# Kernel tuning notes

Hardware: AMD Instinct MI355X
Metric: run time of the kernel (lower is better)

The kernel has to match this reference:

```python
import jax, jax.numpy as jnp
import numpy as np

NEG_INF = -9.0e15  # matches torch's -9000000000000000.0 mask value
ALPHA = 0.2        # leaky_relu negative slope
F_OUT = 128


def setup_inputs() -> dict:
    key = jax.random.key(0)
    k1, k2, k3, k4 = jax.random.split(key, 4)
    B, N, F_IN = 4, 4096, 128
    x = jax.random.normal(k1, (B, N, F_IN), dtype=jnp.float32)
    adj = jax.random.randint(k2, (B, N, N), 0, 2, dtype=jnp.int32)
    # xavier-uniform-like init for params
    lim_W = float(np.sqrt(6.0 / (F_IN + F_OUT)))
    W = jax.random.uniform(k3, (F_IN, F_OUT), jnp.float32, -lim_W, lim_W)
    lim_a = float(np.sqrt(6.0 / (2 * F_OUT + 1)))
    a = jax.random.uniform(k4, (2 * F_OUT, 1), jnp.float32, -lim_a, lim_a)
    return {"x": x, "adj": adj, "W": W, "a": a}


def reference(x, adj, W, a):
    # x: [B, N, Fin], adj: [B, N, N], W: [Fin, Fout], a: [2*Fout, 1]
    Wh = jnp.matmul(x, W)                       # [B, N, Fout]
    Wh1 = jnp.matmul(Wh, a[:F_OUT, :])          # [B, N, 1]
    Wh2 = jnp.matmul(Wh, a[F_OUT:, :])          # [B, N, 1]
    # NOTE: faithful to the source: e = Wh1 + Wh2 is [B, N, 1] (no transpose)
    e = jax.nn.leaky_relu(Wh1 + Wh2, negative_slope=ALPHA)
    # broadcast e across last dim of adj, mask, row-softmax over axis 2
    scores = jnp.where(adj > 0, e, jnp.float32(NEG_INF))  # [B, N, N]
    attention = jax.nn.softmax(scores, axis=2)
    # dropout with p=0.0 / eval mode -> identity
    h_prime = jnp.matmul(attention, Wh)         # [B, N, Fout]
    return h_prime
```

## Files before the change

kernel.cpp:

```cpp
#include <hip/hip_runtime.h>
#include <hip/hip_bf16.h>

typedef unsigned short u16;
typedef unsigned int u32;
typedef short bf16x8 __attribute__((ext_vector_type(8)));
typedef float f32x4 __attribute__((ext_vector_type(4)));

__device__ inline float bf2f(u16 u) { return __uint_as_float(((u32)u) << 16); }
__device__ inline u16 f2bf(float f) {
    u32 x = __float_as_uint(f);
    return (u16)((x + 0x7FFFu + ((x >> 16) & 1u)) >> 16);
}

__global__ __launch_bounds__(256) void k_gemm1(const float* __restrict__ x,
                                               const float* __restrict__ W,
                                               u16* __restrict__ Wht,
                                               float* __restrict__ S) {
    __shared__ __align__(16) u16 Wt[128][136];
    const int t = threadIdx.x;
    {
        int k = t >> 1;
        int f0 = (t & 1) * 64;
        const float4* wp = reinterpret_cast<const float4*>(W + k * 128 + f0);
#pragma unroll
        for (int q = 0; q < 16; ++q) {
            float4 v = wp[q];
            int f = f0 + q * 4;
            Wt[f + 0][k] = f2bf(v.x);
            Wt[f + 1][k] = f2bf(v.y);
            Wt[f + 2][k] = f2bf(v.z);
            Wt[f + 3][k] = f2bf(v.w);
        }
    }
    __syncthreads();

    const int w = t >> 6, l = t & 63;
    const int lr = l & 15, lg = l >> 4;
    const int fh = (w & 1) * 64;
    const int jh = (w >> 1) * 64;
    const int j0 = blockIdx.x * 128;

    f32x4 acc[4][4];
#pragma unroll
    for (int m = 0; m < 4; ++m)
#pragma unroll
        for (int n = 0; n < 4; ++n) acc[m][n] = (f32x4){0.f, 0.f, 0.f, 0.f};

#pragma unroll
    for (int ks = 0; ks < 4; ++ks) {
        bf16x8 a[4], bb[4];
#pragma unroll
        for (int m = 0; m < 4; ++m)
            a[m] = *reinterpret_cast<const bf16x8*>(&Wt[fh + m * 16 + lr][ks * 32 + lg * 8]);
#pragma unroll
        for (int n = 0; n < 4; ++n) {
            int j = j0 + jh + n * 16 + lr;
            const float* xp = x + (size_t)j * 128 + ks * 32 + lg * 8;
            float4 v0 = *reinterpret_cast<const float4*>(xp);
            float4 v1 = *reinterpret_cast<const float4*>(xp + 4);
            bf16x8 bv;
            bv[0] = (short)f2bf(v0.x); bv[1] = (short)f2bf(v0.y);
            bv[2] = (short)f2bf(v0.z); bv[3] = (short)f2bf(v0.w);
            bv[4] = (short)f2bf(v1.x); bv[5] = (short)f2bf(v1.y);
            bv[6] = (short)f2bf(v1.z); bv[7] = (short)f2bf(v1.w);
            bb[n] = bv;
        }
#pragma unroll
        for (int m = 0; m < 4; ++m)
#pragma unroll
            for (int n = 0; n < 4; ++n)
                acc[m][n] = __builtin_amdgcn_mfma_f32_16x16x32_bf16(a[m], bb[n], acc[m][n], 0, 0, 0);
    }

    const int bb_ = blockIdx.x >> 5;
    const int jj = (blockIdx.x & 31) * 128;
    u16* base = Wht + ((size_t)bb_ << 19);
    float* Sb = S + bb_ * 128;
#pragma unroll
    for (int m = 0; m < 4; ++m) {
        int f = fh + m * 16 + lg * 4;
#pragma unroll
        for (int n = 0; n < 4; ++n) {
            int j = jj + jh + n * 16 + lr;
#pragma unroll
            for (int r = 0; r < 4; ++r)
                base[(size_t)(f + r) * 4096 + j] = f2bf(acc[m][n][r]);
        }
#pragma unroll
        for (int r = 0; r < 4; ++r) {
            float sj = 0.f;
#pragma unroll
            for (int n = 0; n < 4; ++n) sj += acc[m][n][r];
            sj += __shfl_xor(sj, 1);
            sj += __shfl_xor(sj, 2);
            sj += __shfl_xor(sj, 4);
            sj += __shfl_xor(sj, 8);
            if (lr == 0) atomicAdd(&Sb[f + r], sj);
        }
    }
}

__global__ __launch_bounds__(256) void k_gemm2(const int* __restrict__ adj,
                                               const u16* __restrict__ Wht,
                                               float* __restrict__ part,
                                               int* __restrict__ cnt) {
    __shared__ __align__(16) u16 As[2][64][72];

    const int t = threadIdx.x;
    const int raw = blockIdx.x;
    const int swz = (raw & 7) * 64 + (raw >> 3);
    const int b   = swz >> 7;
    const int ksp = (swz >> 6) & 1;
    const int i0  = (swz & 63) * 64;
    const int koff = ksp * 2048;

    const int* adjb = adj + ((size_t)b << 24) + (size_t)i0 * 4096 + koff;
    const u16* whb  = Wht + ((size_t)b << 19) + koff;

    const int ai = t >> 2;
    const int aq = t & 3;
    const int* aptr = adjb + (size_t)ai * 4096 + aq * 16;

    int4 av[4];
    int cntv = 0;

    auto issueA = [&](int kt) {
        const int4* p = reinterpret_cast<const int4*>(aptr + kt * 64);
        av[0] = p[0]; av[1] = p[1]; av[2] = p[2]; av[3] = p[3];
    };
    auto convertA = [&](int buf) {
        u32 u[8];
#pragma unroll
        for (int q = 0; q < 4; ++q) {
            int4 v = av[q];
            cntv += (v.x > 0) + (v.y > 0) + (v.z > 0) + (v.w > 0);
            u[q * 2 + 0] = ((v.x > 0) ? 0x3F80u : 0u) | (((v.y > 0) ? 0x3F80u : 0u) << 16);
            u[q * 2 + 1] = ((v.z > 0) ? 0x3F80u : 0u) | (((v.w > 0) ? 0x3F80u : 0u) << 16);
        }
        *reinterpret_cast<uint4*>(&As[buf][ai][aq * 16]) = make_uint4(u[0], u[1], u[2], u[3]);
        *reinterpret_cast<uint4*>(&As[buf][ai][aq * 16 + 8]) = make_uint4(u[4], u[5], u[6], u[7]);
    };

    const int w = t >> 6, l = t & 63;
    const int lr = l & 15, lg = l >> 4;
    const int ir0 = (w & 1) * 2;
    const int fr0 = (w >> 1) * 4;

    const u16* bptr0 = whb + (size_t)((fr0 + 0) * 16 + lr) * 4096 + lg * 8;
    const u16* bptr1 = whb + (size_t)((fr0 + 1) * 16 + lr) * 4096 + lg * 8;
    const u16* bptr2 = whb + (size_t)((fr0 + 2) * 16 + lr) * 4096 + lg * 8;
    const u16* bptr3 = whb + (size_t)((fr0 + 3) * 16 + lr) * 4096 + lg * 8;

    f32x4 acc[2][4];
#pragma unroll
    for (int m = 0; m < 2; ++m)
#pragma unroll
        for (int n = 0; n < 4; ++n) acc[m][n] = (f32x4){0.f, 0.f, 0.f, 0.f};

    issueA(0);
    convertA(0);
    __syncthreads();

    for (int kt = 0; kt < 32; ++kt) {
        const int cur = kt & 1;
        bf16x8 bb0[4], bb1[4];
        bb0[0] = *reinterpret_cast<const bf16x8*>(bptr0 + kt * 64);
        bb0[1] = *reinterpret_cast<const bf16x8*>(bptr1 + kt * 64);
        bb0[2] = *reinterpret_cast<const bf16x8*>(bptr2 + kt * 64);
        bb0[3] = *reinterpret_cast<const bf16x8*>(bptr3 + kt * 64);
        bb1[0] = *reinterpret_cast<const bf16x8*>(bptr0 + kt * 64 + 32);
        bb1[1] = *reinterpret_cast<const bf16x8*>(bptr1 + kt * 64 + 32);
        bb1[2] = *reinterpret_cast<const bf16x8*>(bptr2 + kt * 64 + 32);
        bb1[3] = *reinterpret_cast<const bf16x8*>(bptr3 + kt * 64 + 32);
        if (kt + 1 < 32) issueA(kt + 1);

#pragma unroll
        for (int ks = 0; ks < 2; ++ks) {
            bf16x8 a0 = *reinterpret_cast<const bf16x8*>(&As[cur][(ir0 + 0) * 16 + lr][ks * 32 + lg * 8]);
            bf16x8 a1 = *reinterpret_cast<const bf16x8*>(&As[cur][(ir0 + 1) * 16 + lr][ks * 32 + lg * 8]);
#pragma unroll
            for (int n = 0; n < 4; ++n) {
                bf16x8 bv = ks ? bb1[n] : bb0[n];
                acc[0][n] = __builtin_amdgcn_mfma_f32_16x16x32_bf16(a0, bv, acc[0][n], 0, 0, 0);
                acc[1][n] = __builtin_amdgcn_mfma_f32_16x16x32_bf16(a1, bv, acc[1][n], 0, 0, 0);
            }
        }

        if (kt + 1 < 32) convertA(cur ^ 1);
        __syncthreads();
    }

    int c = cntv + __shfl_xor(cntv, 1);
    c += __shfl_xor(c, 2);
    if ((t & 3) == 0) atomicAdd(&cnt[b * 4096 + i0 + ai], c);

    float* pb = part + ((size_t)ksp << 21) + ((size_t)b * 4096 + i0) * 128;
#pragma unroll
    for (int m = 0; m < 2; ++m) {
#pragma unroll
        for (int n = 0; n < 4; ++n) {
            int f = (fr0 + n) * 16 + lr;
#pragma unroll
            for (int r = 0; r < 4; ++r) {
                int il = (ir0 + m) * 16 + lg * 4 + r;
                pb[(size_t)il * 128 + f] = acc[m][n][r];
            }
        }
    }
}

__global__ __launch_bounds__(256) void k_fin(const float* __restrict__ part,
                                             const int* __restrict__ cnt,
                                             const float* __restrict__ S,
                                             float* __restrict__ out) {
    int e = blockIdx.x * 256 + threadIdx.x;
    int f = e & 127;
    int row = e >> 7;
    int b = row >> 12;
    int c = cnt[row];
    float p = part[e] + part[e + (1 << 21)];
    float v;
    if (c > 0) v = p / (float)c;
    else       v = S[b * 128 + f] * (1.0f / 4096.0f);
    out[e] = v;
}

extern "C" void kernel_launch(void* const* d_in, const int* in_sizes, int n_in,
                              void* d_out, int out_size, void* d_ws, size_t ws_size,
                              hipStream_t stream) {
    const float* x = (const float*)d_in[0];
    const int* adj = (const int*)d_in[1];
    const float* W = (const float*)d_in[2];
    float* out = (float*)d_out;

    char* wsb = (char*)d_ws;
    float* S    = (float*)(wsb);
    int*   cnt  = (int*)(wsb + 4096);
    float* part = (float*)(wsb + (1u << 20));
    u16*   Wht  = (u16*)(wsb + (1u << 25));

    hipMemsetAsync(wsb, 0, 4096 + 65536, stream);
    k_gemm1<<<128, 256, 0, stream>>>(x, W, Wht, S);
    k_gemm2<<<512, 256, 0, stream>>>(adj, Wht, part, cnt);
    k_fin<<<8192, 256, 0, stream>>>(part, cnt, S, out);
}
```

Measured before the change: 413.5 us.

## Deepen gemm2 prefetch pipeline with two-stage A/B register buffering

```diff
diff --git a/kernel.cpp b/kernel.cpp
--- a/kernel.cpp
+++ b/kernel.cpp
@@ -100,10 +100,10 @@
     }
 }
 
-__global__ __launch_bounds__(256) void k_gemm2(const int* __restrict__ adj,
-                                               const u16* __restrict__ Wht,
-                                               float* __restrict__ part,
-                                               int* __restrict__ cnt) {
+__global__ __launch_bounds__(256, 2) void k_gemm2(const int* __restrict__ adj,
+                                                  const u16* __restrict__ Wht,
+                                                  float* __restrict__ part,
+                                                  int* __restrict__ cnt) {
     __shared__ __align__(16) u16 As[2][64][72];
 
     const int t = threadIdx.x;
@@ -121,35 +121,66 @@
     const int aq = t & 3;
     const int* aptr = adjb + (size_t)ai * 4096 + aq * 16;
 
-    int4 av[4];
     int cntv = 0;
-
-    auto issueA = [&](int kt) {
-        const int4* p = reinterpret_cast<const int4*>(aptr + kt * 64);
-        av[0] = p[0]; av[1] = p[1]; av[2] = p[2]; av[3] = p[3];
-    };
-    auto convertA = [&](int buf) {
-        u32 u[8];
-#pragma unroll
-        for (int q = 0; q < 4; ++q) {
-            int4 v = av[q];
-            cntv += (v.x > 0) + (v.y > 0) + (v.z > 0) + (v.w > 0);
-            u[q * 2 + 0] = ((v.x > 0) ? 0x3F80u : 0u) | (((v.y > 0) ? 0x3F80u : 0u) << 16);
-            u[q * 2 + 1] = ((v.z > 0) ? 0x3F80u : 0u) | (((v.w > 0) ? 0x3F80u : 0u) << 16);
-        }
-        *reinterpret_cast<uint4*>(&As[buf][ai][aq * 16]) = make_uint4(u[0], u[1], u[2], u[3]);
-        *reinterpret_cast<uint4*>(&As[buf][ai][aq * 16 + 8]) = make_uint4(u[4], u[5], u[6], u[7]);
-    };
+    int4 av[2][4];
+    bf16x8 Bk0[2][4], Bk1[2][4];
 
     const int w = t >> 6, l = t & 63;
     const int lr = l & 15, lg = l >> 4;
     const int ir0 = (w & 1) * 2;
     const int fr0 = (w >> 1) * 4;
 
-    const u16* bptr0 = whb + (size_t)((fr0 + 0) * 16 + lr) * 4096 + lg * 8;
-    const u16* bptr1 = whb + (size_t)((fr0 + 1) * 16 + lr) * 4096 + lg * 8;
-    const u16* bptr2 = whb + (size_t)((fr0 + 2) * 16 + lr) * 4096 + lg * 8;
-    const u16* bptr3 = whb + (size_t)((fr0 + 3) * 16 + lr) * 4096 + lg * 8;
+    const u16* bp[4];
+#pragma unroll
+    for (int n = 0; n < 4; ++n)
+        bp[n] = whb + (size_t)((fr0 + n) * 16 + lr) * 4096 + lg * 8;
+
+#define ISSUE_A(P, KT)                                                              \
+    {                                                                               \
+        const int4* _p = reinterpret_cast<const int4*>(aptr + (KT) * 64);           \
+        av[P][0] = _p[0]; av[P][1] = _p[1]; av[P][2] = _p[2]; av[P][3] = _p[3];     \
+    }
+#define ISSUE_B(P, KT)                                                              \
+    {                                                                               \
+        _Pragma("unroll")                                                           \
+        for (int n = 0; n < 4; ++n) {                                               \
+            Bk0[P][n] = *reinterpret_cast<const bf16x8*>(bp[n] + (KT) * 64);        \
+            Bk1[P][n] = *reinterpret_cast<const bf16x8*>(bp[n] + (KT) * 64 + 32);   \
+        }                                                                           \
+    }
+#define CONVERT_A(P)                                                                \
+    {                                                                               \
+        u32 u[8];                                                                   \
+        _Pragma("unroll")                                                           \
+        for (int q = 0; q < 4; ++q) {                                               \
+            int4 v = av[P][q];                                                      \
+            cntv += (v.x > 0) + (v.y > 0) + (v.z > 0) + (v.w > 0);                  \
+            u[q * 2 + 0] = ((v.x > 0) ? 0x3F80u : 0u) | (((v.y > 0) ? 0x3F80u : 0u) << 16); \
+            u[q * 2 + 1] = ((v.z > 0) ? 0x3F80u : 0u) | (((v.w > 0) ? 0x3F80u : 0u) << 16); \
+        }                                                                           \
+        *reinterpret_cast<uint4*>(&As[P][ai][aq * 16]) = make_uint4(u[0], u[1], u[2], u[3]); \
+        *reinterpret_cast<uint4*>(&As[P][ai][aq * 16 + 8]) = make_uint4(u[4], u[5], u[6], u[7]); \
+    }
+#define BARRIER()                                                                   \
+    {                                                                               \
+        asm volatile("s_waitcnt lgkmcnt(0)" ::: "memory");                          \
+        __builtin_amdgcn_sched_barrier(0);                                          \
+        __builtin_amdgcn_s_barrier();                                               \
+    }
+#define MFMA_STEP(P)                                                                \
+    {                                                                               \
+        _Pragma("unroll")                                                           \
+        for (int ks = 0; ks < 2; ++ks) {                                            \
+            bf16x8 a0 = *reinterpret_cast<const bf16x8*>(&As[P][(ir0 + 0) * 16 + lr][ks * 32 + lg * 8]); \
+            bf16x8 a1 = *reinterpret_cast<const bf16x8*>(&As[P][(ir0 + 1) * 16 + lr][ks * 32 + lg * 8]); \
+            _Pragma("unroll")                                                       \
+            for (int n = 0; n < 4; ++n) {                                           \
+                bf16x8 bv = ks ? Bk1[P][n] : Bk0[P][n];                             \
+                acc[0][n] = __builtin_amdgcn_mfma_f32_16x16x32_bf16(a0, bv, acc[0][n], 0, 0, 0); \
+                acc[1][n] = __builtin_amdgcn_mfma_f32_16x16x32_bf16(a1, bv, acc[1][n], 0, 0, 0); \
+            }                                                                       \
+        }                                                                           \
+    }
 
     f32x4 acc[2][4];
 #pragma unroll
@@ -157,38 +188,36 @@
 #pragma unroll
         for (int n = 0; n < 4; ++n) acc[m][n] = (f32x4){0.f, 0.f, 0.f, 0.f};
 
-    issueA(0);
-    convertA(0);
-    __syncthreads();
-
-    for (int kt = 0; kt < 32; ++kt) {
-        const int cur = kt & 1;
-        bf16x8 bb0[4], bb1[4];
-        bb0[0] = *reinterpret_cast<const bf16x8*>(bptr0 + kt * 64);
-        bb0[1] = *reinterpret_cast<const bf16x8*>(bptr1 + kt * 64);
-        bb0[2] = *reinterpret_cast<const bf16x8*>(bptr2 + kt * 64);
-        bb0[3] = *reinterpret_cast<const bf16x8*>(bptr3 + kt * 64);
-        bb1[0] = *reinterpret_cast<const bf16x8*>(bptr0 + kt * 64 + 32);
-        bb1[1] = *reinterpret_cast<const bf16x8*>(bptr1 + kt * 64 + 32);
-        bb1[2] = *reinterpret_cast<const bf16x8*>(bptr2 + kt * 64 + 32);
-        bb1[3] = *reinterpret_cast<const bf16x8*>(bptr3 + kt * 64 + 32);
-        if (kt + 1 < 32) issueA(kt + 1);
-
-#pragma unroll
-        for (int ks = 0; ks < 2; ++ks) {
-            bf16x8 a0 = *reinterpret_cast<const bf16x8*>(&As[cur][(ir0 + 0) * 16 + lr][ks * 32 + lg * 8]);
-            bf16x8 a1 = *reinterpret_cast<const bf16x8*>(&As[cur][(ir0 + 1) * 16 + lr][ks * 32 + lg * 8]);
-#pragma unroll
-            for (int n = 0; n < 4; ++n) {
-                bf16x8 bv = ks ? bb1[n] : bb0[n];
-                acc[0][n] = __builtin_amdgcn_mfma_f32_16x16x32_bf16(a0, bv, acc[0][n], 0, 0, 0);
-                acc[1][n] = __builtin_amdgcn_mfma_f32_16x16x32_bf16(a1, bv, acc[1][n], 0, 0, 0);
-            }
-        }
-
-        if (kt + 1 < 32) convertA(cur ^ 1);
-        __syncthreads();
-    }
+    ISSUE_A(0, 0);
+    ISSUE_A(1, 1);
+    CONVERT_A(0);
+    ISSUE_B(0, 0);
+    BARRIER();
+
+    for (int kp = 0; kp < 15; ++kp) {
+        const int kt0 = kp * 2;
+        ISSUE_A(0, kt0 + 2);
+        ISSUE_B(1, kt0 + 1);
+        MFMA_STEP(0);
+        CONVERT_A(1);
+        BARRIER();
+        ISSUE_A(1, kt0 + 3);
+        ISSUE_B(0, kt0 + 2);
+        MFMA_STEP(1);
+        CONVERT_A(0);
+        BARRIER();
+    }
+    ISSUE_B(1, 31);
+    MFMA_STEP(0);
+    CONVERT_A(1);
+    BARRIER();
+    MFMA_STEP(1);
+
+#undef ISSUE_A
+#undef ISSUE_B
+#undef CONVERT_A
+#undef BARRIER
+#undef MFMA_STEP
 
     int c = cntv + __shfl_xor(cntv, 1);
     c += __shfl_xor(c, 2);
@@ -237,7 +266,7 @@
     float* S    = (float*)(wsb);
     int*   cnt  = (int*)(wsb + 4096);
     float* part = (float*)(wsb + (1u << 20));
-    u16*   Wht  = (u16*)(wsb + (1u << 25));
+    u16*   Wht  = (u16*)(wsb + (40u << 20));
 
     hipMemsetAsync(wsb, 0, 4096 + 65536, stream);
     k_gemm1<<<128, 256, 0, stream>>>(x, W, Wht, S);
```

Result: no change. 413.7 us (+0.0%).

## Load adjacency straight into MFMA registers, dropping LDS staging in gemm2

Applied to the files above, without the earlier changes.

```diff
diff --git a/kernel.cpp b/kernel.cpp
--- a/kernel.cpp
+++ b/kernel.cpp
@@ -100,12 +100,21 @@
     }
 }
 
-__global__ __launch_bounds__(256) void k_gemm2(const int* __restrict__ adj,
-                                               const u16* __restrict__ Wht,
-                                               float* __restrict__ part,
-                                               int* __restrict__ cnt) {
-    __shared__ __align__(16) u16 As[2][64][72];
-
+__device__ inline bf16x8 conv8(int4 a, int4 b, int& c) {
+    c += (a.x > 0) + (a.y > 0) + (a.z > 0) + (a.w > 0)
+       + (b.x > 0) + (b.y > 0) + (b.z > 0) + (b.w > 0);
+    u32 u0 = ((a.x > 0) ? 0x3F80u : 0u) | (((a.y > 0) ? 0x3F80u : 0u) << 16);
+    u32 u1 = ((a.z > 0) ? 0x3F80u : 0u) | (((a.w > 0) ? 0x3F80u : 0u) << 16);
+    u32 u2 = ((b.x > 0) ? 0x3F80u : 0u) | (((b.y > 0) ? 0x3F80u : 0u) << 16);
+    u32 u3 = ((b.z > 0) ? 0x3F80u : 0u) | (((b.w > 0) ? 0x3F80u : 0u) << 16);
+    uint4 q = make_uint4(u0, u1, u2, u3);
+    return __builtin_bit_cast(bf16x8, q);
+}
+
+__global__ __launch_bounds__(256, 2) void k_gemm2(const int* __restrict__ adj,
+                                                  const u16* __restrict__ Wht,
+                                                  float* __restrict__ part,
+                                                  int* __restrict__ cnt) {
     const int t = threadIdx.x;
     const int raw = blockIdx.x;
     const int swz = (raw & 7) * 64 + (raw >> 3);
@@ -114,97 +123,77 @@
     const int i0  = (swz & 63) * 64;
     const int koff = ksp * 2048;
 
-    const int* adjb = adj + ((size_t)b << 24) + (size_t)i0 * 4096 + koff;
-    const u16* whb  = Wht + ((size_t)b << 19) + koff;
-
-    const int ai = t >> 2;
-    const int aq = t & 3;
-    const int* aptr = adjb + (size_t)ai * 4096 + aq * 16;
-
-    int4 av[4];
-    int cntv = 0;
-
-    auto issueA = [&](int kt) {
-        const int4* p = reinterpret_cast<const int4*>(aptr + kt * 64);
-        av[0] = p[0]; av[1] = p[1]; av[2] = p[2]; av[3] = p[3];
-    };
-    auto convertA = [&](int buf) {
-        u32 u[8];
-#pragma unroll
-        for (int q = 0; q < 4; ++q) {
-            int4 v = av[q];
-            cntv += (v.x > 0) + (v.y > 0) + (v.z > 0) + (v.w > 0);
-            u[q * 2 + 0] = ((v.x > 0) ? 0x3F80u : 0u) | (((v.y > 0) ? 0x3F80u : 0u) << 16);
-            u[q * 2 + 1] = ((v.z > 0) ? 0x3F80u : 0u) | (((v.w > 0) ? 0x3F80u : 0u) << 16);
-        }
-        *reinterpret_cast<uint4*>(&As[buf][ai][aq * 16]) = make_uint4(u[0], u[1], u[2], u[3]);
-        *reinterpret_cast<uint4*>(&As[buf][ai][aq * 16 + 8]) = make_uint4(u[4], u[5], u[6], u[7]);
-    };
-
     const int w = t >> 6, l = t & 63;
     const int lr = l & 15, lg = l >> 4;
-    const int ir0 = (w & 1) * 2;
-    const int fr0 = (w >> 1) * 4;
-
-    const u16* bptr0 = whb + (size_t)((fr0 + 0) * 16 + lr) * 4096 + lg * 8;
-    const u16* bptr1 = whb + (size_t)((fr0 + 1) * 16 + lr) * 4096 + lg * 8;
-    const u16* bptr2 = whb + (size_t)((fr0 + 2) * 16 + lr) * 4096 + lg * 8;
-    const u16* bptr3 = whb + (size_t)((fr0 + 3) * 16 + lr) * 4096 + lg * 8;
-
-    f32x4 acc[2][4];
-#pragma unroll
-    for (int m = 0; m < 2; ++m)
-#pragma unroll
-        for (int n = 0; n < 4; ++n) acc[m][n] = (f32x4){0.f, 0.f, 0.f, 0.f};
-
-    issueA(0);
-    convertA(0);
-    __syncthreads();
-
-    for (int kt = 0; kt < 32; ++kt) {
-        const int cur = kt & 1;
-        bf16x8 bb0[4], bb1[4];
-        bb0[0] = *reinterpret_cast<const bf16x8*>(bptr0 + kt * 64);
-        bb0[1] = *reinterpret_cast<const bf16x8*>(bptr1 + kt * 64);
-        bb0[2] = *reinterpret_cast<const bf16x8*>(bptr2 + kt * 64);
-        bb0[3] = *reinterpret_cast<const bf16x8*>(bptr3 + kt * 64);
-        bb1[0] = *reinterpret_cast<const bf16x8*>(bptr0 + kt * 64 + 32);
-        bb1[1] = *reinterpret_cast<const bf16x8*>(bptr1 + kt * 64 + 32);
-        bb1[2] = *reinterpret_cast<const bf16x8*>(bptr2 + kt * 64 + 32);
-        bb1[3] = *reinterpret_cast<const bf16x8*>(bptr3 + kt * 64 + 32);
-        if (kt + 1 < 32) issueA(kt + 1);
-
-#pragma unroll
-        for (int ks = 0; ks < 2; ++ks) {
-            bf16x8 a0 = *reinterpret_cast<const bf16x8*>(&As[cur][(ir0 + 0) * 16 + lr][ks * 32 + lg * 8]);
-            bf16x8 a1 = *reinterpret_cast<const bf16x8*>(&As[cur][(ir0 + 1) * 16 + lr][ks * 32 + lg * 8]);
-#pragma unroll
-            for (int n = 0; n < 4; ++n) {
-                bf16x8 bv = ks ? bb1[n] : bb0[n];
-                acc[0][n] = __builtin_amdgcn_mfma_f32_16x16x32_bf16(a0, bv, acc[0][n], 0, 0, 0);
-                acc[1][n] = __builtin_amdgcn_mfma_f32_16x16x32_bf16(a1, bv, acc[1][n], 0, 0, 0);
-            }
-        }
-
-        if (kt + 1 < 32) convertA(cur ^ 1);
-        __syncthreads();
-    }
-
-    int c = cntv + __shfl_xor(cntv, 1);
-    c += __shfl_xor(c, 2);
-    if ((t & 3) == 0) atomicAdd(&cnt[b * 4096 + i0 + ai], c);
+    const int arow = i0 + w * 16 + lr;
+
+    const int* apn = adj + ((size_t)b << 24) + (size_t)arow * 4096 + koff + lg * 8;
+    const u16* whb = Wht + ((size_t)b << 19) + koff;
+
+    const u16* bq[8];
+#pragma unroll
+    for (int n = 0; n < 8; ++n)
+        bq[n] = whb + (size_t)(n * 16 + lr) * 4096 + lg * 8;
+
+    int4 av[2][4];
+    int cntv = 0;
+    f32x4 acc[8];
+#pragma unroll
+    for (int n = 0; n < 8; ++n) acc[n] = (f32x4){0.f, 0.f, 0.f, 0.f};
+
+#define ISSUE_A(P)                                                   \
+    {                                                                \
+        const int4* _p = reinterpret_cast<const int4*>(apn);         \
+        av[P][0] = _p[0]; av[P][1] = _p[1];      \
+        av[P][2] = _p[8]; av[P][3] = _p[9];   \
+        apn += 64;                                                   \
+    }
+
+#define STEP(P, DO_ISSUE)                                                         \
+    {                                                                             \
+        bf16x8 a0 = conv8(av[P][0], av[P][1], cntv);                              \
+        bf16x8 a1 = conv8(av[P][2], av[P][3], cntv);                              \
+        if (DO_ISSUE) ISSUE_A(P);                                                 \
+        bf16x8 b0[8], b1[8];                                                      \
+        _Pragma("unroll")                                                         \
+        for (int n = 0; n < 8; ++n) b0[n] = *reinterpret_cast<const bf16x8*>(bq[n]);      \
+        _Pragma("unroll")                                                         \
+        for (int n = 0; n < 8; ++n) b1[n] = *reinterpret_cast<const bf16x8*>(bq[n] + 32); \
+        _Pragma("unroll")                                                         \
+        for (int n = 0; n < 8; ++n)                                               \
+            acc[n] = __builtin_amdgcn_mfma_f32_16x16x32_bf16(a0, b0[n], acc[n], 0, 0, 0); \
+        _Pragma("unroll")                                                         \
+        for (int n = 0; n < 8; ++n)                                               \
+            acc[n] = __builtin_amdgcn_mfma_f32_16x16x32_bf16(a1, b1[n], acc[n], 0, 0, 0); \
+        _Pragma("unroll")                                                         \
+        for (int n = 0; n < 8; ++n) bq[n] += 64;                                  \
+    }
+
+    ISSUE_A(0);
+    ISSUE_A(1);
+
+    for (int kp = 0; kp < 15; ++kp) {
+        STEP(0, 1);
+        STEP(1, 1);
+    }
+    STEP(0, 0);
+    STEP(1, 0);
+
+#undef ISSUE_A
+#undef STEP
+
+    int c = cntv + __shfl_xor(cntv, 16);
+    c += __shfl_xor(c, 32);
+    if (lg == 0) atomicAdd(&cnt[b * 4096 + i0 + w * 16 + lr], c);
 
     float* pb = part + ((size_t)ksp << 21) + ((size_t)b * 4096 + i0) * 128;
 #pragma unroll
-    for (int m = 0; m < 2; ++m) {
-#pragma unroll
-        for (int n = 0; n < 4; ++n) {
-            int f = (fr0 + n) * 16 + lr;
-#pragma unroll
-            for (int r = 0; r < 4; ++r) {
-                int il = (ir0 + m) * 16 + lg * 4 + r;
-                pb[(size_t)il * 128 + f] = acc[m][n][r];
-            }
+    for (int n = 0; n < 8; ++n) {
+        int f = n * 16 + lr;
+#pragma unroll
+        for (int r = 0; r < 4; ++r) {
+            int il = w * 16 + lg * 4 + r;
+            pb[(size_t)il * 128 + f] = acc[n][r];
         }
     }
 }
@@ -237,7 +226,7 @@
     float* S    = (float*)(wsb);
     int*   cnt  = (int*)(wsb + 4096);
     float* part = (float*)(wsb + (1u << 20));
-    u16*   Wht  = (u16*)(wsb + (1u << 25));
+    u16*   Wht  = (u16*)(wsb + (40u << 20));
 
     hipMemsetAsync(wsb, 0, 4096 + 65536, stream);
     k_gemm1<<<128, 256, 0, stream>>>(x, W, Wht, S);
```

Result: slower. 480.2 us (+16.1%).
